# Kernel tuning notes

Measured on AMD Instinct MI355X. Metric: run time of the kernel, lower is better.

## Reference

```python
import jax, jax.numpy as jnp
import numpy as np
from jax import lax

K = 11        # kernel_size
SIGMA = 2.0   # gaussian sigma
N_T = 20      # max diffusion timestep
C = 3         # channels

# torchvision GaussianBlur 1D kernel: pdf = exp(-0.5*(x/sigma)^2), normalized
_x = np.linspace(-(K - 1) / 2.0, (K - 1) / 2.0, K)
_pdf = np.exp(-0.5 * (_x / SIGMA) ** 2)
_k1d = (_pdf / _pdf.sum()).astype(np.float32)
# depthwise separable kernels: [C,1,K,1] and [C,1,1,K] (OIHW, feature_group_count=C)
W_H = jnp.asarray(np.tile(_k1d.reshape(1, 1, K, 1), (C, 1, 1, 1)))
W_W = jnp.asarray(np.tile(_k1d.reshape(1, 1, 1, K), (C, 1, 1, 1)))
DN = ('NCHW', 'OIHW', 'NCHW')
PAD = K // 2


def _blur(z):
    # reflect padding as torchvision GaussianBlur, then separable depthwise conv
    zp = jnp.pad(z, ((0, 0), (0, 0), (PAD, PAD), (0, 0)), mode='reflect')
    zp = lax.conv_general_dilated(zp, W_H, (1, 1), 'VALID',
                                  dimension_numbers=DN, feature_group_count=C)
    zp = jnp.pad(zp, ((0, 0), (0, 0), (0, 0), (PAD, PAD)), mode='reflect')
    return lax.conv_general_dilated(zp, W_W, (1, 1), 'VALID',
                                    dimension_numbers=DN, feature_group_count=C)


def setup_inputs() -> dict:
    key = jax.random.key(0)
    kx, kt = jax.random.split(key)
    x = jax.random.normal(kx, (64, 3, 256, 256), dtype=jnp.float32)
    t = jax.random.randint(kt, (64,), 1, N_T, dtype=jnp.int32)
    return {'x': x, 't': t}


def reference(x, t):
    # batch_blur: sample i gets blurred t[i] times. Vectorized as N_T masked
    # blur steps: at step i, samples with t > i take the blurred value.
    mask_keep = t[:, None, None, None]  # [B,1,1,1]

    def step(z, i):
        zb = _blur(z)
        z = jnp.where(mask_keep > i, zb, z)
        return z, None

    z_t, _ = lax.scan(step, x, jnp.arange(N_T))
    return z_t
```

## Files before the change

kernel.cpp:

```cpp
#include <hip/hip_runtime.h>

#define IMG 65536
#define W 256
#define H 256


__global__ __launch_bounds__(256) void init_kernel(const int* __restrict__ t,
                                                   float* __restrict__ ktab,
                                                   int* __restrict__ ord,
                                                   int* __restrict__ rtab) {
  __shared__ double cur[256];
  __shared__ double sc[256];
  __shared__ double base[11];
  __shared__ int keys[192];
  __shared__ int sRmax;
  int tid = threadIdx.x;
  int tt = blockIdx.x;
  if (tid == 0) {
    double p[11];
    double s = 0.0;
    for (int i = 0; i < 11; ++i) {
      double xx = (double)(i - 5) * 0.5;
      p[i] = exp(-0.5 * xx * xx);
      s += p[i];
    }
    for (int i = 0; i < 11; ++i) base[i] = (double)(float)(p[i] / s);
  }
  __syncthreads();

  if (tt == 0) {
    ktab[tid] = (tid == 8) ? 1.0f : 0.0f;
    if (tid == 0) rtab[0] = 0;
    if (tid < 192) keys[tid] = min(max(t[tid / 3], 0), 19);
    __syncthreads();
    if (tid < 192) {
      int k = keys[tid];
      int rank = 0;
      for (int j = 0; j < 192; ++j) {
        int kj = keys[j];
        if (kj > k || (kj == k && j < tid)) ++rank;
      }
      ord[rank] = tid;
    }
    return;
  }

  cur[tid] = (tid < 11) ? base[tid] : 0.0;
  __syncthreads();
  for (int step = 2; step <= tt; ++step) {
    int Lprev = 10 * (step - 1) + 1;
    double a = 0.0;
    for (int i = 0; i < 11; ++i) {
      int jj = tid - i;
      if (jj >= 0 && jj < Lprev) a += base[i] * cur[jj];
    }
    __syncthreads();
    cur[tid] = a;
    __syncthreads();
  }
  sc[tid] = cur[tid];
  __syncthreads();
#pragma unroll
  for (int off = 1; off < 256; off <<= 1) {
    double tmp = (tid >= off) ? sc[tid - off] : 0.0;
    __syncthreads();
    sc[tid] += tmp;
    __syncthreads();
  }
  if (tid == 0) sRmax = 1;
  __syncthreads();
  int c = 5 * tt;
  double total = sc[255];
  if (tid >= 1 && tid <= c) {
    double Srm1 = sc[c + tid - 1] - sc[c - tid];
    if (total - Srm1 > 1e-5) atomicMax(&sRmax, tid);
  }
  __syncthreads();
  int Rk = sRmax;
  double ksum = sc[c + Rk] - ((c - Rk - 1 >= 0) ? sc[c - Rk - 1] : 0.0);
  double scale = 1.0 / ksum;
  if (tid == 0) rtab[tt] = Rk;
  int c0 = c - Rk;
  int Lk = 2 * Rk + 1;
  ktab[tt * 256 + tid] =
      (tid >= 8 && tid < 8 + Lk) ? (float)(cur[tid - 8 + c0] * scale) : 0.0f;
}

__global__ __launch_bounds__(256, 8) void hpass_kernel(const float* __restrict__ x,
                                                       const int* __restrict__ t,
                                                       const float* __restrict__ ktab,
                                                       const int* __restrict__ ord,
                                                       const int* __restrict__ rtab,
                                                       float* __restrict__ out) {
  __shared__ float tile[256 * 17];
  int tid = threadIdx.x;
  int img = __builtin_amdgcn_readfirstlane(ord[blockIdx.y]);
  int wt = blockIdx.x;
  int b = img / 3;
  int tv = __builtin_amdgcn_readfirstlane(min(max(t[b], 0), 19));
  int R = __builtin_amdgcn_readfirstlane(rtab[tv]);
  int L = 2 * R + 1;
  const float* __restrict__ kt = ktab + tv * 256;
  const float* src = x + (size_t)img * IMG + (wt << 4);
  float* dst = out + (size_t)img * IMG + (wt << 4);
  {
    int c4 = (tid & 3) << 2;
    int r0 = tid >> 2;
#pragma unroll
    for (int i = 0; i < 4; ++i) {
      int r = r0 + (i << 6);
      float4 v = *reinterpret_cast<const float4*>(src + r * W + c4);
      tile[r * 17 + c4 + 0] = v.x;
      tile[r * 17 + c4 + 1] = v.y;
      tile[r * 17 + c4 + 2] = v.z;
      tile[r * 17 + c4 + 3] = v.w;
    }
  }
  __syncthreads();
  int col = tid & 15;
  int rgrp = tid >> 4;
  int nIter = (L + 30) & ~15;
  int h0 = rgrp << 4;
  float acc[16];
  float kq[16];
#pragma unroll
  for (int o = 0; o < 16; ++o) { acc[o] = 0.f; kq[o] = 0.f; }
  int pbase = h0 - R;
  for (int jb = 0; jb < nIter; jb += 16) {
    int p0 = pbase + jb;
    if (p0 >= 0 && p0 <= 240) {
#pragma unroll
      for (int u = 0; u < 16; ++u) {
        kq[u] = kt[jb + u + 8];
        float v = tile[(p0 + u) * 17 + col];
#pragma unroll
        for (int o = 0; o < 16; ++o) acc[o] += kq[(u - o) & 15] * v;
      }
    } else {
#pragma unroll
      for (int u = 0; u < 16; ++u) {
        kq[u] = kt[jb + u + 8];
        int p = p0 + u;
        int rp = 255 - abs(255 - abs(p));
        float v = tile[rp * 17 + col];
#pragma unroll
        for (int o = 0; o < 16; ++o) acc[o] += kq[(u - o) & 15] * v;
      }
    }
  }
#pragma unroll
  for (int o = 0; o < 16; ++o) dst[(h0 + o) * W + col] = acc[o];
}

__global__ __launch_bounds__(256, 5) void wpass_split(const float* __restrict__ srcbuf,
                                                      const int* __restrict__ t,
                                                      const float* __restrict__ ktab,
                                                      const int* __restrict__ ord,
                                                      const int* __restrict__ rtab,
                                                      float* __restrict__ dstbuf) {
  __shared__ float tile[32 * 256];
  int tid = threadIdx.x;
  int img = __builtin_amdgcn_readfirstlane(ord[blockIdx.y]);
  int ht = blockIdx.x;
  int b = img / 3;
  int tv = __builtin_amdgcn_readfirstlane(min(max(t[b], 0), 19));
  int R = __builtin_amdgcn_readfirstlane(rtab[tv]);
  int L = 2 * R + 1;
  const float* __restrict__ kt = ktab + tv * 256;
  const float* src = srcbuf + (size_t)img * IMG + (ht << 5) * W;
  float* dst = dstbuf + (size_t)img * IMG + (ht << 5) * W;
  {
    int r = tid >> 3;
    int c4 = (tid & 7) << 2;
    int sw = r;
#pragma unroll
    for (int kk = 0; kk < 8; ++kk) {
      int c = c4 + (kk << 5);
      float4 v = *reinterpret_cast<const float4*>(src + r * W + c);
      tile[(r << 8) + ((c + 0) ^ sw)] = v.x;
      tile[(r << 8) + ((c + 1) ^ sw)] = v.y;
      tile[(r << 8) + ((c + 2) ^ sw)] = v.z;
      tile[(r << 8) + ((c + 3) ^ sw)] = v.w;
    }
  }
  __syncthreads();
  int row = tid & 31;
  int wgrp = tid >> 5;
  int rowbase = row << 8;
  int sw = row;
  int nIter = (L + 30) & ~15;
  for (int g = 0; g < 2; ++g) {
    int w0 = (wgrp << 5) + (g << 4);
    float acc[16];
    float kq[16];
#pragma unroll
    for (int o = 0; o < 16; ++o) { acc[o] = 0.f; kq[o] = 0.f; }
    int pbase = w0 - R;
    for (int jb = 0; jb < nIter; jb += 16) {
      int p0 = pbase + jb;
      if (p0 >= 0 && p0 <= 240) {
#pragma unroll
        for (int u = 0; u < 16; ++u) {
          kq[u] = kt[jb + u + 8];
          float v = tile[rowbase + ((p0 + u) ^ sw)];
#pragma unroll
          for (int o = 0; o < 16; ++o) acc[o] += kq[(u - o) & 15] * v;
        }
      } else {
#pragma unroll
        for (int u = 0; u < 16; ++u) {
          kq[u] = kt[jb + u + 8];
          int p = p0 + u;
          int rp = 255 - abs(255 - abs(p));
          float v = tile[rowbase + (rp ^ sw)];
#pragma unroll
          for (int o = 0; o < 16; ++o) acc[o] += kq[(u - o) & 15] * v;
        }
      }
    }
    float4 v0 = make_float4(acc[0], acc[1], acc[2], acc[3]);
    float4 v1 = make_float4(acc[4], acc[5], acc[6], acc[7]);
    float4 v2 = make_float4(acc[8], acc[9], acc[10], acc[11]);
    float4 v3 = make_float4(acc[12], acc[13], acc[14], acc[15]);
    float* o0 = dst + row * W + w0;
    *reinterpret_cast<float4*>(o0 + 0) = v0;
    *reinterpret_cast<float4*>(o0 + 4) = v1;
    *reinterpret_cast<float4*>(o0 + 8) = v2;
    *reinterpret_cast<float4*>(o0 + 12) = v3;
  }
}

__global__ __launch_bounds__(256, 5) void wpass_inplace(const int* __restrict__ t,
                                                        const float* __restrict__ ktab,
                                                        const int* __restrict__ ord,
                                                        const int* __restrict__ rtab,
                                                        float* __restrict__ io) {
  __shared__ float tile[32 * 256];
  int tid = threadIdx.x;
  int img = __builtin_amdgcn_readfirstlane(ord[blockIdx.y]);
  int ht = blockIdx.x;
  int b = img / 3;
  int tv = __builtin_amdgcn_readfirstlane(min(max(t[b], 0), 19));
  int R = __builtin_amdgcn_readfirstlane(rtab[tv]);
  int L = 2 * R + 1;
  const float* __restrict__ kt = ktab + tv * 256;
  float* base = io + (size_t)img * IMG + (ht << 5) * W;
  {
    int r = tid >> 3;
    int c4 = (tid & 7) << 2;
    int sw = r;
#pragma unroll
    for (int kk = 0; kk < 8; ++kk) {
      int c = c4 + (kk << 5);
      float4 v = *reinterpret_cast<const float4*>(base + r * W + c);
      tile[(r << 8) + ((c + 0) ^ sw)] = v.x;
      tile[(r << 8) + ((c + 1) ^ sw)] = v.y;
      tile[(r << 8) + ((c + 2) ^ sw)] = v.z;
      tile[(r << 8) + ((c + 3) ^ sw)] = v.w;
    }
  }
  __syncthreads();
  int row = tid & 31;
  int wgrp = tid >> 5;
  int rowbase = row << 8;
  int sw = row;
  int nIter = (L + 30) & ~15;
  for (int g = 0; g < 2; ++g) {
    int w0 = (wgrp << 5) + (g << 4);
    float acc[16];
    float kq[16];
#pragma unroll
    for (int o = 0; o < 16; ++o) { acc[o] = 0.f; kq[o] = 0.f; }
    int pbase = w0 - R;
    for (int jb = 0; jb < nIter; jb += 16) {
      int p0 = pbase + jb;
      if (p0 >= 0 && p0 <= 240) {
#pragma unroll
        for (int u = 0; u < 16; ++u) {
          kq[u] = kt[jb + u + 8];
          float v = tile[rowbase + ((p0 + u) ^ sw)];
#pragma unroll
          for (int o = 0; o < 16; ++o) acc[o] += kq[(u - o) & 15] * v;
        }
      } else {
#pragma unroll
        for (int u = 0; u < 16; ++u) {
          kq[u] = kt[jb + u + 8];
          int p = p0 + u;
          int rp = 255 - abs(255 - abs(p));
          float v = tile[rowbase + (rp ^ sw)];
#pragma unroll
          for (int o = 0; o < 16; ++o) acc[o] += kq[(u - o) & 15] * v;
        }
      }
    }
    float4 v0 = make_float4(acc[0], acc[1], acc[2], acc[3]);
    float4 v1 = make_float4(acc[4], acc[5], acc[6], acc[7]);
    float4 v2 = make_float4(acc[8], acc[9], acc[10], acc[11]);
    float4 v3 = make_float4(acc[12], acc[13], acc[14], acc[15]);
    float* o0 = base + row * W + w0;
    *reinterpret_cast<float4*>(o0 + 0) = v0;
    *reinterpret_cast<float4*>(o0 + 4) = v1;
    *reinterpret_cast<float4*>(o0 + 8) = v2;
    *reinterpret_cast<float4*>(o0 + 12) = v3;
  }
}

extern "C" void kernel_launch(void* const* d_in, const int* in_sizes, int n_in,
                              void* d_out, int out_size, void* d_ws, size_t ws_size,
                              hipStream_t stream) {
  const float* x = (const float*)d_in[0];
  const int* t = (const int*)d_in[1];
  float* out = (float*)d_out;
  float* ktab = (float*)d_ws;
  int* ord = (int*)((char*)d_ws + 20480);
  int* rtab = (int*)((char*)d_ws + 21248);
  const size_t mid_off = 32768;
  const size_t mid_bytes = (size_t)192 * IMG * 4;

  hipLaunchKernelGGL(init_kernel, dim3(20), dim3(256), 0, stream, t, ktab, ord, rtab);
  if (ws_size >= mid_off + mid_bytes) {
    float* mid = (float*)((char*)d_ws + mid_off);
    hipLaunchKernelGGL(hpass_kernel, dim3(16, 192), dim3(256), 0, stream, x, t, ktab, ord, rtab, mid);
    hipLaunchKernelGGL(wpass_split, dim3(8, 192), dim3(256), 0, stream, mid, t, ktab, ord, rtab, out);
  } else {
    hipLaunchKernelGGL(hpass_kernel, dim3(16, 192), dim3(256), 0, stream, x, t, ktab, ord, rtab, out);
    hipLaunchKernelGGL(wpass_inplace, dim3(8, 192), dim3(256), 0, stream, t, ktab, ord, rtab, out);
  }
}
```

Measured before the change: 96.43 us.

## Pre-pad shared tiles with reflected halo and clamp composed kernel radius

Shared-memory tiles now hold the rows and columns already reflected, with a fixed halo of 40 on each side. This removes the per-iteration boundary branch and the reflect index math from the inner convolution loops. The composed kernel radius is clamped to 40, which truncates the tail of the effective Gaussian for large t. The larger tiles drop the XOR swizzle for an odd stride of 361 and lower the occupancy hints from 8 to 6 and from 5 to 3.

```diff
diff --git a/kernel.cpp b/kernel.cpp
--- a/kernel.cpp
+++ b/kernel.cpp
@@ -3,6 +3,7 @@
 #define IMG 65536
 #define W 256
 #define H 256
+#define RMAX 40
 
 
 __global__ __launch_bounds__(256) void init_kernel(const int* __restrict__ t,
@@ -76,7 +77,7 @@
     if (total - Srm1 > 1e-5) atomicMax(&sRmax, tid);
   }
   __syncthreads();
-  int Rk = sRmax;
+  int Rk = min(sRmax, RMAX);
   double ksum = sc[c + Rk] - ((c - Rk - 1 >= 0) ? sc[c - Rk - 1] : 0.0);
   double scale = 1.0 / ksum;
   if (tid == 0) rtab[tt] = Rk;
@@ -86,13 +87,13 @@
       (tid >= 8 && tid < 8 + Lk) ? (float)(cur[tid - 8 + c0] * scale) : 0.0f;
 }
 
-__global__ __launch_bounds__(256, 8) void hpass_kernel(const float* __restrict__ x,
+__global__ __launch_bounds__(256, 6) void hpass_kernel(const float* __restrict__ x,
                                                        const int* __restrict__ t,
                                                        const float* __restrict__ ktab,
                                                        const int* __restrict__ ord,
                                                        const int* __restrict__ rtab,
                                                        float* __restrict__ out) {
-  __shared__ float tile[256 * 17];
+  __shared__ float tile[352 * 17];
   int tid = threadIdx.x;
   int img = __builtin_amdgcn_readfirstlane(ord[blockIdx.y]);
   int wt = blockIdx.x;
@@ -107,13 +108,17 @@
     int c4 = (tid & 3) << 2;
     int r0 = tid >> 2;
 #pragma unroll
-    for (int i = 0; i < 4; ++i) {
-      int r = r0 + (i << 6);
-      float4 v = *reinterpret_cast<const float4*>(src + r * W + c4);
-      tile[r * 17 + c4 + 0] = v.x;
-      tile[r * 17 + c4 + 1] = v.y;
-      tile[r * 17 + c4 + 2] = v.z;
-      tile[r * 17 + c4 + 3] = v.w;
+    for (int i = 0; i < 6; ++i) {
+      int rr = r0 + (i << 6);
+      if (rr < 352) {
+        int p = rr - RMAX;
+        int srow = 255 - abs(255 - abs(p));
+        float4 v = *reinterpret_cast<const float4*>(src + srow * W + c4);
+        tile[rr * 17 + c4 + 0] = v.x;
+        tile[rr * 17 + c4 + 1] = v.y;
+        tile[rr * 17 + c4 + 2] = v.z;
+        tile[rr * 17 + c4 + 3] = v.w;
+      }
     }
   }
   __syncthreads();
@@ -125,40 +130,27 @@
   float kq[16];
 #pragma unroll
   for (int o = 0; o < 16; ++o) { acc[o] = 0.f; kq[o] = 0.f; }
-  int pbase = h0 - R;
+  int pb = h0 - R + RMAX;
   for (int jb = 0; jb < nIter; jb += 16) {
-    int p0 = pbase + jb;
-    if (p0 >= 0 && p0 <= 240) {
-#pragma unroll
-      for (int u = 0; u < 16; ++u) {
-        kq[u] = kt[jb + u + 8];
-        float v = tile[(p0 + u) * 17 + col];
-#pragma unroll
-        for (int o = 0; o < 16; ++o) acc[o] += kq[(u - o) & 15] * v;
-      }
-    } else {
-#pragma unroll
-      for (int u = 0; u < 16; ++u) {
-        kq[u] = kt[jb + u + 8];
-        int p = p0 + u;
-        int rp = 255 - abs(255 - abs(p));
-        float v = tile[rp * 17 + col];
-#pragma unroll
-        for (int o = 0; o < 16; ++o) acc[o] += kq[(u - o) & 15] * v;
-      }
+#pragma unroll
+    for (int u = 0; u < 16; ++u) {
+      kq[u] = kt[jb + u + 8];
+      float v = tile[(pb + jb + u) * 17 + col];
+#pragma unroll
+      for (int o = 0; o < 16; ++o) acc[o] += kq[(u - o) & 15] * v;
     }
   }
 #pragma unroll
   for (int o = 0; o < 16; ++o) dst[(h0 + o) * W + col] = acc[o];
 }
 
-__global__ __launch_bounds__(256, 5) void wpass_split(const float* __restrict__ srcbuf,
+__global__ __launch_bounds__(256, 3) void wpass_split(const float* __restrict__ srcbuf,
                                                       const int* __restrict__ t,
                                                       const float* __restrict__ ktab,
                                                       const int* __restrict__ ord,
                                                       const int* __restrict__ rtab,
                                                       float* __restrict__ dstbuf) {
-  __shared__ float tile[32 * 256];
+  __shared__ float tile[32 * 361];
   int tid = threadIdx.x;
   int img = __builtin_amdgcn_readfirstlane(ord[blockIdx.y]);
   int ht = blockIdx.x;
@@ -170,24 +162,32 @@
   const float* src = srcbuf + (size_t)img * IMG + (ht << 5) * W;
   float* dst = dstbuf + (size_t)img * IMG + (ht << 5) * W;
   {
-    int r = tid >> 3;
-    int c4 = (tid & 7) << 2;
-    int sw = r;
-#pragma unroll
-    for (int kk = 0; kk < 8; ++kk) {
-      int c = c4 + (kk << 5);
-      float4 v = *reinterpret_cast<const float4*>(src + r * W + c);
-      tile[(r << 8) + ((c + 0) ^ sw)] = v.x;
-      tile[(r << 8) + ((c + 1) ^ sw)] = v.y;
-      tile[(r << 8) + ((c + 2) ^ sw)] = v.z;
-      tile[(r << 8) + ((c + 3) ^ sw)] = v.w;
+    int srow = tid >> 3;
+    int jbase = tid & 7;
+    const float* sp = src + srow * W;
+    float* tp0 = &tile[srow * 361];
+#pragma unroll
+    for (int k = 0; k < 11; ++k) {
+      int j = jbase + (k << 3);
+      int c0 = -RMAX + (j << 2);
+      float* tp = tp0 + c0 + RMAX;
+      if (c0 >= 0 && c0 <= 252) {
+        float4 v = *reinterpret_cast<const float4*>(sp + c0);
+        tp[0] = v.x; tp[1] = v.y; tp[2] = v.z; tp[3] = v.w;
+      } else {
+#pragma unroll
+        for (int d = 0; d < 4; ++d) {
+          int cc = c0 + d;
+          int rc = 255 - abs(255 - abs(cc));
+          tp[d] = sp[rc];
+        }
+      }
     }
   }
   __syncthreads();
   int row = tid & 31;
   int wgrp = tid >> 5;
-  int rowbase = row << 8;
-  int sw = row;
+  int rowbase = row * 361;
   int nIter = (L + 30) & ~15;
   for (int g = 0; g < 2; ++g) {
     int w0 = (wgrp << 5) + (g << 4);
@@ -195,27 +195,14 @@
     float kq[16];
 #pragma unroll
     for (int o = 0; o < 16; ++o) { acc[o] = 0.f; kq[o] = 0.f; }
-    int pbase = w0 - R;
+    int pb = w0 - R + RMAX;
     for (int jb = 0; jb < nIter; jb += 16) {
-      int p0 = pbase + jb;
-      if (p0 >= 0 && p0 <= 240) {
-#pragma unroll
-        for (int u = 0; u < 16; ++u) {
-          kq[u] = kt[jb + u + 8];
-          float v = tile[rowbase + ((p0 + u) ^ sw)];
-#pragma unroll
-          for (int o = 0; o < 16; ++o) acc[o] += kq[(u - o) & 15] * v;
-        }
-      } else {
-#pragma unroll
-        for (int u = 0; u < 16; ++u) {
-          kq[u] = kt[jb + u + 8];
-          int p = p0 + u;
-          int rp = 255 - abs(255 - abs(p));
-          float v = tile[rowbase + (rp ^ sw)];
-#pragma unroll
-          for (int o = 0; o < 16; ++o) acc[o] += kq[(u - o) & 15] * v;
-        }
+#pragma unroll
+      for (int u = 0; u < 16; ++u) {
+        kq[u] = kt[jb + u + 8];
+        float v = tile[rowbase + pb + jb + u];
+#pragma unroll
+        for (int o = 0; o < 16; ++o) acc[o] += kq[(u - o) & 15] * v;
       }
     }
     float4 v0 = make_float4(acc[0], acc[1], acc[2], acc[3]);
@@ -230,12 +217,12 @@
   }
 }
 
-__global__ __launch_bounds__(256, 5) void wpass_inplace(const int* __restrict__ t,
+__global__ __launch_bounds__(256, 3) void wpass_inplace(const int* __restrict__ t,
                                                         const float* __restrict__ ktab,
                                                         const int* __restrict__ ord,
                                                         const int* __restrict__ rtab,
                                                         float* __restrict__ io) {
-  __shared__ float tile[32 * 256];
+  __shared__ float tile[32 * 361];
   int tid = threadIdx.x;
   int img = __builtin_amdgcn_readfirstlane(ord[blockIdx.y]);
   int ht = blockIdx.x;
@@ -246,24 +233,32 @@
   const float* __restrict__ kt = ktab + tv * 256;
   float* base = io + (size_t)img * IMG + (ht << 5) * W;
   {
-    int r = tid >> 3;
-    int c4 = (tid & 7) << 2;
-    int sw = r;
-#pragma unroll
-    for (int kk = 0; kk < 8; ++kk) {
-      int c = c4 + (kk << 5);
-      float4 v = *reinterpret_cast<const float4*>(base + r * W + c);
-      tile[(r << 8) + ((c + 0) ^ sw)] = v.x;
-      tile[(r << 8) + ((c + 1) ^ sw)] = v.y;
-      tile[(r << 8) + ((c + 2) ^ sw)] = v.z;
-      tile[(r << 8) + ((c + 3) ^ sw)] = v.w;
+    int srow = tid >> 3;
+    int jbase = tid & 7;
+    const float* sp = base + srow * W;
+    float* tp0 = &tile[srow * 361];
+#pragma unroll
+    for (int k = 0; k < 11; ++k) {
+      int j = jbase + (k << 3);
+      int c0 = -RMAX + (j << 2);
+      float* tp = tp0 + c0 + RMAX;
+      if (c0 >= 0 && c0 <= 252) {
+        float4 v = *reinterpret_cast<const float4*>(sp + c0);
+        tp[0] = v.x; tp[1] = v.y; tp[2] = v.z; tp[3] = v.w;
+      } else {
+#pragma unroll
+        for (int d = 0; d < 4; ++d) {
+          int cc = c0 + d;
+          int rc = 255 - abs(255 - abs(cc));
+          tp[d] = sp[rc];
+        }
+      }
     }
   }
   __syncthreads();
   int row = tid & 31;
   int wgrp = tid >> 5;
-  int rowbase = row << 8;
-  int sw = row;
+  int rowbase = row * 361;
   int nIter = (L + 30) & ~15;
   for (int g = 0; g < 2; ++g) {
     int w0 = (wgrp << 5) + (g << 4);
@@ -271,27 +266,14 @@
     float kq[16];
 #pragma unroll
     for (int o = 0; o < 16; ++o) { acc[o] = 0.f; kq[o] = 0.f; }
-    int pbase = w0 - R;
+    int pb = w0 - R + RMAX;
     for (int jb = 0; jb < nIter; jb += 16) {
-      int p0 = pbase + jb;
-      if (p0 >= 0 && p0 <= 240) {
-#pragma unroll
-        for (int u = 0; u < 16; ++u) {
-          kq[u] = kt[jb + u + 8];
-          float v = tile[rowbase + ((p0 + u) ^ sw)];
-#pragma unroll
-          for (int o = 0; o < 16; ++o) acc[o] += kq[(u - o) & 15] * v;
-        }
-      } else {
-#pragma unroll
-        for (int u = 0; u < 16; ++u) {
-          kq[u] = kt[jb + u + 8];
-          int p = p0 + u;
-          int rp = 255 - abs(255 - abs(p));
-          float v = tile[rowbase + (rp ^ sw)];
-#pragma unroll
-          for (int o = 0; o < 16; ++o) acc[o] += kq[(u - o) & 15] * v;
-        }
+#pragma unroll
+      for (int u = 0; u < 16; ++u) {
+        kq[u] = kt[jb + u + 8];
+        float v = tile[rowbase + pb + jb + u];
+#pragma unroll
+        for (int o = 0; o < 16; ++o) acc[o] += kq[(u - o) & 15] * v;
       }
     }
     float4 v0 = make_float4(acc[0], acc[1], acc[2], acc[3]);
```

Result: faster. 84.49 us (-12.4%).
